# Optimization experiments

Measured on AMD Instinct MI355X. Metric: run time of the kernel, lower is better.

The kernel has to match this reference:

```python
import jax, jax.numpy as jnp
import numpy as np

HEAD = 8
PAD = (2, 2)   # (mod//2, mod//2 + mod%2) for dim=508, head=8 -> mod=4
EPS = 1e-6


def setup_inputs() -> dict:
    key = jax.random.key(0)
    ks = jax.random.split(key, 4)
    d_pad = 512  # 508 + mod(4)
    s = 1.0 / np.sqrt(d_pad).astype(np.float32)
    inp = jax.random.normal(ks[0], (2, 2048, 508), dtype=jnp.float32)
    Wq = jax.random.normal(ks[1], (d_pad, d_pad), dtype=jnp.float32) * s
    Wk = jax.random.normal(ks[2], (d_pad, d_pad), dtype=jnp.float32) * s
    Wv = jax.random.normal(ks[3], (d_pad, d_pad), dtype=jnp.float32) * s
    gamma = jnp.ones((d_pad,), dtype=jnp.float32)
    beta = jnp.zeros((d_pad,), dtype=jnp.float32)
    return {"inp": inp, "Wq": Wq, "Wk": Wk, "Wv": Wv, "gamma": gamma, "beta": beta}


def reference(inp, Wq, Wk, Wv, gamma, beta):
    # pad feature dim so it divides head count (torch F.pad on last dim)
    x = jnp.pad(inp, ((0, 0), (0, 0), (PAD[0], PAD[1])))  # [B, L, D]
    residual = x
    b, l, d = x.shape
    h = HEAD
    dh = d // h
    inv_sqrt_dh = 1.0 / np.sqrt(dh).astype(np.float32)

    def proj(W):
        # torch Linear (no bias): x @ W.T ; then split heads -> [B, H, L, dh]
        return (x @ W.T).reshape(b, l, h, dh).transpose(0, 2, 1, 3)

    q = proj(Wq)
    k = proj(Wk)
    v = proj(Wv)

    score = jnp.einsum('bhld,bhmd->bhlm', q, k) * inv_sqrt_dh  # [B,H,L,L]
    attn = jax.nn.softmax(score, axis=-1)
    out = jnp.einsum('bhlm,bhmd->bhld', attn, v)               # [B,H,L,dh]
    out = out.transpose(0, 2, 1, 3).reshape(b, l, d)           # unshape

    # dropout is identity in eval mode; residual + layernorm
    y = out + residual
    mu = jnp.mean(y, axis=-1, keepdims=True)
    var = jnp.mean(jnp.square(y - mu), axis=-1, keepdims=True)
    z = (y - mu) / jnp.sqrt(var + EPS)
    out = gamma * z + beta

    out = out[:, :, PAD[0]:-PAD[1]]  # strip padding back to original dim
    return out, attn
```

## Files before the change

kernel.cpp:

```cpp
#include <hip/hip_runtime.h>

typedef short bf16x8 __attribute__((ext_vector_type(8)));
typedef float f32x4 __attribute__((ext_vector_type(4)));
typedef unsigned short u16;
typedef u16 u16x8 __attribute__((ext_vector_type(8)));
typedef u16 u16x4 __attribute__((ext_vector_type(4)));

#define L_ 2048
#define D_ 512
#define H_ 8
#define DH_ 64
#define DIN 508
#define EXPC 0.18033688011112042f

static __device__ __forceinline__ u16 f2b(float f){
  unsigned u = __builtin_bit_cast(unsigned, f);
  unsigned r = u + 0x7fffu + ((u >> 16) & 1u);
  return (u16)(r >> 16);
}
static __device__ __forceinline__ float b2f(u16 u){
  unsigned x = ((unsigned)u) << 16;
  return __builtin_bit_cast(float, x);
}
static __device__ __forceinline__ bf16x8 asbf(u16x8 v){
  return __builtin_bit_cast(bf16x8, v);
}
#define MFMA16(a,b,c) __builtin_amdgcn_mfma_f32_16x16x32_bf16(a,b,c,0,0,0)

__global__ __launch_bounds__(512) void cvt_kernel(
    const float* __restrict__ inp, const float* __restrict__ Wq,
    const float* __restrict__ Wk, const float* __restrict__ Wv,
    u16* __restrict__ Xb, u16* __restrict__ Wb)
{
  const int tid = blockIdx.x*512 + threadIdx.x;
  if (tid < 262144) {
    const int idx8 = tid*8;
    const int row = idx8 >> 9, col = idx8 & 511;
    u16x8 o;
    #pragma unroll
    for (int e=0;e<8;++e){
      const int c = col+e;
      const float v = (c>=2 && c<510) ? inp[(size_t)row*DIN + (c-2)] : 0.f;
      o[e] = f2b(v);
    }
    *(u16x8*)&Xb[idx8] = o;
  } else {
    const int idx8 = (tid - 262144)*8;
    const int row = idx8 >> 9, col = idx8 & 511;
    const float* __restrict__ W = (row < 512) ? Wq : (row < 1024) ? Wk : Wv;
    const float* p = &W[(size_t)(row & 511)*D_ + col];
    u16x8 o;
    #pragma unroll
    for (int e=0;e<8;++e) o[e] = f2b(p[e]);
    *(u16x8*)&Wb[idx8] = o;
  }
}

__global__ __launch_bounds__(512) void proj_kernel(
    const u16* __restrict__ Xb, const u16* __restrict__ Wb,
    u16* __restrict__ Qg, u16* __restrict__ Kg, u16* __restrict__ Vt)
{
  __shared__ u16 Xl[128*72];
  __shared__ u16 Wl[128*72];
  const int t = threadIdx.x;
  const int lane = t & 63, wid = t >> 6;
  const int wr = wid >> 2, wc = wid & 3;
  const int i0 = blockIdx.x * 128;
  const int j0 = blockIdx.y * 128;
  const int mat = j0 >> 9;
  const int srow = t >> 3, sc8 = (t & 7) * 8;

  f32x4 acc[4][2];
  #pragma unroll
  for (int a=0;a<4;++a){
    #pragma unroll
    for (int bq=0;bq<2;++bq){ f32x4 z = {0.f,0.f,0.f,0.f}; acc[a][bq] = z; }
  }

  u16x8 xa0 = *(const u16x8*)&Xb[(size_t)(i0+srow)*D_ + sc8];
  u16x8 xa1 = *(const u16x8*)&Xb[(size_t)(i0+64+srow)*D_ + sc8];
  u16x8 wa0 = *(const u16x8*)&Wb[(size_t)(j0+srow)*D_ + sc8];
  u16x8 wa1 = *(const u16x8*)&Wb[(size_t)(j0+64+srow)*D_ + sc8];

  for (int kt=0; kt<8; ++kt){
    __syncthreads();
    *(u16x8*)&Xl[srow*72 + sc8] = xa0;
    *(u16x8*)&Xl[(64+srow)*72 + sc8] = xa1;
    *(u16x8*)&Wl[srow*72 + sc8] = wa0;
    *(u16x8*)&Wl[(64+srow)*72 + sc8] = wa1;
    __syncthreads();
    if (kt < 7){
      const int k1 = (kt+1)*64;
      xa0 = *(const u16x8*)&Xb[(size_t)(i0+srow)*D_ + k1 + sc8];
      xa1 = *(const u16x8*)&Xb[(size_t)(i0+64+srow)*D_ + k1 + sc8];
      wa0 = *(const u16x8*)&Wb[(size_t)(j0+srow)*D_ + k1 + sc8];
      wa1 = *(const u16x8*)&Wb[(size_t)(j0+64+srow)*D_ + k1 + sc8];
    }
    #pragma unroll
    for (int ks=0; ks<2; ++ks){
      const int ko = ks*32 + (lane>>4)*8;
      bf16x8 af[4], bfr[2];
      #pragma unroll
      for (int fm=0; fm<4; ++fm)
        af[fm] = *(const bf16x8*)&Xl[(wr*64 + fm*16 + (lane&15))*72 + ko];
      #pragma unroll
      for (int fn=0; fn<2; ++fn)
        bfr[fn] = *(const bf16x8*)&Wl[(wc*32 + fn*16 + (lane&15))*72 + ko];
      #pragma unroll
      for (int fm=0; fm<4; ++fm){
        #pragma unroll
        for (int fn=0; fn<2; ++fn)
          acc[fm][fn] = MFMA16(af[fm], bfr[fn], acc[fm][fn]);
      }
    }
  }
  #pragma unroll
  for (int fm=0; fm<4; ++fm){
    const int ibase = i0 + wr*64 + fm*16 + (lane>>4)*4;
    const int b = ibase >> 11;
    const int li = ibase & (L_-1);
    #pragma unroll
    for (int fn=0; fn<2; ++fn){
      const int n = j0 + wc*32 + fn*16 + (lane&15);
      const int h = (n>>6) & 7;
      const int dh = n & 63;
      if (mat == 2){
        u16x4 pk;
        #pragma unroll
        for (int r=0;r<4;++r) pk[r] = f2b(acc[fm][fn][r]);
        *(u16x4*)&Vt[((size_t)(b*H_+h)*DH_ + dh)*L_ + li] = pk;
      } else {
        u16* dst = ((mat==0)? Qg : Kg) + ((size_t)(b*H_+h)*L_ + li)*DH_ + dh;
        #pragma unroll
        for (int r=0;r<4;++r) dst[(size_t)r*DH_] = f2b(acc[fm][fn][r]);
      }
    }
  }
}

__global__ __launch_bounds__(512, 4) void attn_kernel(
    const u16* __restrict__ Qg, const u16* __restrict__ Kg,
    const u16* __restrict__ Vt, float* __restrict__ attn, float* __restrict__ Og)
{
  __shared__ u16 Vbuf[2][64*136];
  __shared__ u16 Pbuf[2][32*136];
  __shared__ float inv_rs[32];
  float* rsp = (float*)Vbuf;

  const int t = threadIdx.x, lane = t & 63, wid = t >> 6;
  const int lane15 = lane & 15, g = lane >> 4, g4 = g*8;
  const int lin = blockIdx.x;
  const int idx = lin >> 3;
  const int bh = (lin & 7) + 8*(idx & 1);
  const int q0 = (idx >> 1) * 32;
  const u16* Qp = Qg + ((size_t)bh*L_ + q0)*DH_;
  const u16* Kp = Kg + (size_t)bh*L_*DH_;
  const u16* Vp = Vt + (size_t)bh*DH_*L_;

  bf16x8 qf[2][2];
  #pragma unroll
  for (int qi=0;qi<2;++qi){
    #pragma unroll
    for (int ks=0;ks<2;++ks)
      qf[qi][ks] = *(const bf16x8*)&Qp[(size_t)(qi*16 + lane15)*DH_ + ks*32 + g4];
  }

  const int vr0 = t>>4, vcm = (t&15)*8;
  const int mrow = wid*16 + lane15;

  float racc0 = 0.f, racc1 = 0.f;
  {
    u16x8 nk0 = *(const u16x8*)&Kp[(size_t)mrow*DH_ + g4];
    u16x8 nk1 = *(const u16x8*)&Kp[(size_t)mrow*DH_ + 32 + g4];
    for (int kt=0; kt<16; ++kt){
      bf16x8 kf0 = asbf(nk0), kf1 = asbf(nk1);
      if (kt < 15){
        nk0 = *(const u16x8*)&Kp[(size_t)((kt+1)*128 + mrow)*DH_ + g4];
        nk1 = *(const u16x8*)&Kp[(size_t)((kt+1)*128 + mrow)*DH_ + 32 + g4];
      }
      f32x4 s0 = {0.f,0.f,0.f,0.f}, s1 = {0.f,0.f,0.f,0.f};
      s0 = MFMA16(kf0, qf[0][0], s0); s0 = MFMA16(kf1, qf[0][1], s0);
      s1 = MFMA16(kf0, qf[1][0], s1); s1 = MFMA16(kf1, qf[1][1], s1);
      #pragma unroll
      for (int r=0;r<4;++r){
        racc0 += exp2f(s0[r]*EXPC);
        racc1 += exp2f(s1[r]*EXPC);
      }
    }
  }
  racc0 += __shfl_xor(racc0, 16); racc0 += __shfl_xor(racc0, 32);
  racc1 += __shfl_xor(racc1, 16); racc1 += __shfl_xor(racc1, 32);
  if (lane < 16){ rsp[wid*32 + lane] = racc0; rsp[wid*32 + 16 + lane] = racc1; }
  __syncthreads();
  if (t < 32){
    float s = 0.f;
    #pragma unroll
    for (int w=0;w<8;++w) s += rsp[w*32 + t];
    inv_rs[t] = 1.f/s;
  }
  __syncthreads();

  const int qpv = wid>>2, d0 = (wid&3)*16;
  f32x4 o0 = {0.f,0.f,0.f,0.f}, o1 = {0.f,0.f,0.f,0.f};
  const int sr = t >> 4;
  const int sc4 = (t & 15) * 4;
  float* abase = attn + ((size_t)bh*L_ + q0 + sr)*L_ + sc4;
  const float sinv = inv_rs[sr];

  u16x8 k0 = *(const u16x8*)&Kp[(size_t)mrow*DH_ + g4];
  u16x8 k1 = *(const u16x8*)&Kp[(size_t)mrow*DH_ + 32 + g4];
  u16x8 va = *(const u16x8*)&Vp[(size_t)vr0*L_ + vcm];
  u16x8 vb = *(const u16x8*)&Vp[(size_t)(32+vr0)*L_ + vcm];

  {
    f32x4 s0 = {0.f,0.f,0.f,0.f}, s1 = {0.f,0.f,0.f,0.f};
    s0 = MFMA16(asbf(k0), qf[0][0], s0); s0 = MFMA16(asbf(k1), qf[0][1], s0);
    s1 = MFMA16(asbf(k0), qf[1][0], s1); s1 = MFMA16(asbf(k1), qf[1][1], s1);
    u16x4 p0, p1;
    #pragma unroll
    for (int r=0;r<4;++r){ p0[r] = f2b(exp2f(s0[r]*EXPC)); p1[r] = f2b(exp2f(s1[r]*EXPC)); }
    *(u16x4*)&Pbuf[0][lane15*136 + wid*16 + g*4] = p0;
    *(u16x4*)&Pbuf[0][(16 + lane15)*136 + wid*16 + g*4] = p1;
    *(u16x8*)&Vbuf[0][vr0*136 + vcm] = va;
    *(u16x8*)&Vbuf[0][(32+vr0)*136 + vcm] = vb;
  }
  __syncthreads();

  for (int kt=0; kt<16; ++kt){
    const int cur = kt & 1;
    if (kt < 15){
      k0 = *(const u16x8*)&Kp[(size_t)((kt+1)*128 + mrow)*DH_ + g4];
      k1 = *(const u16x8*)&Kp[(size_t)((kt+1)*128 + mrow)*DH_ + 32 + g4];
      va = *(const u16x8*)&Vp[(size_t)vr0*L_ + (kt+1)*128 + vcm];
      vb = *(const u16x8*)&Vp[(size_t)(32+vr0)*L_ + (kt+1)*128 + vcm];
    }
    {
      const u16x4 pva = *(const u16x4*)&Pbuf[cur][sr*136 + sc4];
      const u16x4 pvb = *(const u16x4*)&Pbuf[cur][sr*136 + 64 + sc4];
      f32x4 w0, w1;
      w0[0]=b2f(pva[0])*sinv; w0[1]=b2f(pva[1])*sinv;
      w0[2]=b2f(pva[2])*sinv; w0[3]=b2f(pva[3])*sinv;
      w1[0]=b2f(pvb[0])*sinv; w1[1]=b2f(pvb[1])*sinv;
      w1[2]=b2f(pvb[2])*sinv; w1[3]=b2f(pvb[3])*sinv;
      __builtin_nontemporal_store(w0, (f32x4*)&abase[kt*128]);
      __builtin_nontemporal_store(w1, (f32x4*)&abase[kt*128 + 64]);
    }
    #pragma unroll
    for (int ms=0; ms<4; ++ms){
      bf16x8 pa = *(const bf16x8*)&Pbuf[cur][(qpv*16 + lane15)*136 + ms*32 + g4];
      bf16x8 vv = *(const bf16x8*)&Vbuf[cur][(d0 + lane15)*136 + ms*32 + g4];
      if (ms&1) o1 = MFMA16(pa, vv, o1); else o0 = MFMA16(pa, vv, o0);
    }
    if (kt < 15){
      f32x4 s0 = {0.f,0.f,0.f,0.f}, s1 = {0.f,0.f,0.f,0.f};
      s0 = MFMA16(asbf(k0), qf[0][0], s0); s0 = MFMA16(asbf(k1), qf[0][1], s0);
      s1 = MFMA16(asbf(k0), qf[1][0], s1); s1 = MFMA16(asbf(k1), qf[1][1], s1);
      u16x4 p0, p1;
      #pragma unroll
      for (int r=0;r<4;++r){ p0[r] = f2b(exp2f(s0[r]*EXPC)); p1[r] = f2b(exp2f(s1[r]*EXPC)); }
      *(u16x4*)&Pbuf[cur^1][lane15*136 + wid*16 + g*4] = p0;
      *(u16x4*)&Pbuf[cur^1][(16 + lane15)*136 + wid*16 + g*4] = p1;
      *(u16x8*)&Vbuf[cur^1][vr0*136 + vcm] = va;
      *(u16x8*)&Vbuf[cur^1][(32+vr0)*136 + vcm] = vb;
    }
    __syncthreads();
  }
  {
    const int b = bh>>3, h = bh&7;
    #pragma unroll
    for (int r=0;r<4;++r){
      const int qr = qpv*16 + g*4 + r;
      Og[((size_t)(b*L_ + q0 + qr))*D_ + h*DH_ + d0 + lane15] = (o0[r]+o1[r])*inv_rs[qr];
    }
  }
}

__global__ __launch_bounds__(256) void ln_kernel(
    const float* __restrict__ Og, const float* __restrict__ inp,
    const float* __restrict__ gamma, const float* __restrict__ beta,
    float* __restrict__ out0)
{
  const int row = blockIdx.x, t = threadIdx.x;
  const int lane = t & 63, wid = t >> 6;
  const int c2 = t + 256;
  const float x1 = (t >= 2) ? inp[(size_t)row*DIN + t-2] : 0.f;
  const float x2 = (c2 < 510) ? inp[(size_t)row*DIN + c2-2] : 0.f;
  const float y1 = Og[(size_t)row*D_ + t]  + x1;
  const float y2 = Og[(size_t)row*D_ + c2] + x2;
  float s = y1 + y2, ss = y1*y1 + y2*y2;
  #pragma unroll
  for (int off=1; off<64; off<<=1){
    s  += __shfl_xor(s,  off);
    ss += __shfl_xor(ss, off);
  }
  __shared__ float red[4][2];
  if (lane == 0){ red[wid][0] = s; red[wid][1] = ss; }
  __syncthreads();
  s  = red[0][0]+red[1][0]+red[2][0]+red[3][0];
  ss = red[0][1]+red[1][1]+red[2][1]+red[3][1];
  const float mu   = s * (1.f/512.f);
  const float var  = ss * (1.f/512.f) - mu*mu;
  const float rstd = rsqrtf(var + 1e-6f);
  const float z1 = (y1 - mu)*rstd*gamma[t]  + beta[t];
  const float z2 = (y2 - mu)*rstd*gamma[c2] + beta[c2];
  if (t >= 2)   out0[(size_t)row*DIN + t-2]  = z1;
  if (c2 < 510) out0[(size_t)row*DIN + c2-2] = z2;
}

extern "C" void kernel_launch(void* const* d_in, const int* in_sizes, int n_in,
                              void* d_out, int out_size, void* d_ws, size_t ws_size,
                              hipStream_t stream) {
  const float* inp   = (const float*)d_in[0];
  const float* Wq    = (const float*)d_in[1];
  const float* Wk    = (const float*)d_in[2];
  const float* Wv    = (const float*)d_in[3];
  const float* gamma = (const float*)d_in[4];
  const float* beta  = (const float*)d_in[5];

  char* ws = (char*)d_ws;
  u16*   Qg = (u16*)(ws);
  u16*   Kg = (u16*)(ws + 4194304);
  u16*   Vt = (u16*)(ws + 8388608);
  float* Og = (float*)(ws + 12582912);
  u16*   Xb = (u16*)(ws + 12582912);
  u16*   Wb = (u16*)(ws + 16777216);

  float* out0 = (float*)d_out;
  float* attn = out0 + 2080768;

  cvt_kernel <<<704, 512, 0, stream>>>(inp, Wq, Wk, Wv, Xb, Wb);
  proj_kernel<<<dim3(32,12), 512, 0, stream>>>(Xb, Wb, Qg, Kg, Vt);
  attn_kernel<<<1024, 512, 0, stream>>>(Qg, Kg, Vt, attn, Og);
  ln_kernel  <<<4096, 256, 0, stream>>>(Og, inp, gamma, beta, out0);
}
```

Baseline: 132.6 us.

## Batch attention-probability stores into 512-column chunks with a wider P staging buffer

Replaces the double-buffered 128-column P and V tiles with a single 32x512 P staging buffer and one V tile. The normalized attention weights are written to global memory once every four key tiles, each warp storing four full rows of 512 columns. The goal is longer contiguous nontemporal store runs for the large attn output. In exchange the software pipelining between score computation and PV is lost, and each iteration now needs two or three barriers.

```diff
diff --git a/kernel.cpp b/kernel.cpp
--- a/kernel.cpp
+++ b/kernel.cpp
@@ -142,10 +142,10 @@
     const u16* __restrict__ Qg, const u16* __restrict__ Kg,
     const u16* __restrict__ Vt, float* __restrict__ attn, float* __restrict__ Og)
 {
-  __shared__ u16 Vbuf[2][64*136];
-  __shared__ u16 Pbuf[2][32*136];
+  __shared__ u16 P4[32*520];
+  __shared__ u16 Vl[64*136];
   __shared__ float inv_rs[32];
-  float* rsp = (float*)Vbuf;
+  float* rsp = (float*)P4;
 
   const int t = threadIdx.x, lane = t & 63, wid = t >> 6;
   const int lane15 = lane & 15, g = lane >> 4, g4 = g*8;
@@ -202,68 +202,59 @@
 
   const int qpv = wid>>2, d0 = (wid&3)*16;
   f32x4 o0 = {0.f,0.f,0.f,0.f}, o1 = {0.f,0.f,0.f,0.f};
-  const int sr = t >> 4;
-  const int sc4 = (t & 15) * 4;
-  float* abase = attn + ((size_t)bh*L_ + q0 + sr)*L_ + sc4;
-  const float sinv = inv_rs[sr];
 
   u16x8 k0 = *(const u16x8*)&Kp[(size_t)mrow*DH_ + g4];
   u16x8 k1 = *(const u16x8*)&Kp[(size_t)mrow*DH_ + 32 + g4];
   u16x8 va = *(const u16x8*)&Vp[(size_t)vr0*L_ + vcm];
   u16x8 vb = *(const u16x8*)&Vp[(size_t)(32+vr0)*L_ + vcm];
 
-  {
-    f32x4 s0 = {0.f,0.f,0.f,0.f}, s1 = {0.f,0.f,0.f,0.f};
-    s0 = MFMA16(asbf(k0), qf[0][0], s0); s0 = MFMA16(asbf(k1), qf[0][1], s0);
-    s1 = MFMA16(asbf(k0), qf[1][0], s1); s1 = MFMA16(asbf(k1), qf[1][1], s1);
-    u16x4 p0, p1;
-    #pragma unroll
-    for (int r=0;r<4;++r){ p0[r] = f2b(exp2f(s0[r]*EXPC)); p1[r] = f2b(exp2f(s1[r]*EXPC)); }
-    *(u16x4*)&Pbuf[0][lane15*136 + wid*16 + g*4] = p0;
-    *(u16x4*)&Pbuf[0][(16 + lane15)*136 + wid*16 + g*4] = p1;
-    *(u16x8*)&Vbuf[0][vr0*136 + vcm] = va;
-    *(u16x8*)&Vbuf[0][(32+vr0)*136 + vcm] = vb;
-  }
-  __syncthreads();
-
   for (int kt=0; kt<16; ++kt){
-    const int cur = kt & 1;
+    const int cbase = (kt & 3) * 128;
+    bf16x8 kf0 = asbf(k0), kf1 = asbf(k1);
     if (kt < 15){
       k0 = *(const u16x8*)&Kp[(size_t)((kt+1)*128 + mrow)*DH_ + g4];
       k1 = *(const u16x8*)&Kp[(size_t)((kt+1)*128 + mrow)*DH_ + 32 + g4];
+    }
+    f32x4 s0 = {0.f,0.f,0.f,0.f}, s1 = {0.f,0.f,0.f,0.f};
+    s0 = MFMA16(kf0, qf[0][0], s0); s0 = MFMA16(kf1, qf[0][1], s0);
+    s1 = MFMA16(kf0, qf[1][0], s1); s1 = MFMA16(kf1, qf[1][1], s1);
+    u16x4 p0, p1;
+    #pragma unroll
+    for (int r=0;r<4;++r){ p0[r] = f2b(exp2f(s0[r]*EXPC)); p1[r] = f2b(exp2f(s1[r]*EXPC)); }
+    *(u16x4*)&P4[lane15*520 + cbase + wid*16 + g*4] = p0;
+    *(u16x4*)&P4[(16 + lane15)*520 + cbase + wid*16 + g*4] = p1;
+    __syncthreads();
+    *(u16x8*)&Vl[vr0*136 + vcm] = va;
+    *(u16x8*)&Vl[(32+vr0)*136 + vcm] = vb;
+    if (kt < 15){
       va = *(const u16x8*)&Vp[(size_t)vr0*L_ + (kt+1)*128 + vcm];
       vb = *(const u16x8*)&Vp[(size_t)(32+vr0)*L_ + (kt+1)*128 + vcm];
     }
-    {
-      const u16x4 pva = *(const u16x4*)&Pbuf[cur][sr*136 + sc4];
-      const u16x4 pvb = *(const u16x4*)&Pbuf[cur][sr*136 + 64 + sc4];
-      f32x4 w0, w1;
-      w0[0]=b2f(pva[0])*sinv; w0[1]=b2f(pva[1])*sinv;
-      w0[2]=b2f(pva[2])*sinv; w0[3]=b2f(pva[3])*sinv;
-      w1[0]=b2f(pvb[0])*sinv; w1[1]=b2f(pvb[1])*sinv;
-      w1[2]=b2f(pvb[2])*sinv; w1[3]=b2f(pvb[3])*sinv;
-      __builtin_nontemporal_store(w0, (f32x4*)&abase[kt*128]);
-      __builtin_nontemporal_store(w1, (f32x4*)&abase[kt*128 + 64]);
-    }
+    __syncthreads();
     #pragma unroll
     for (int ms=0; ms<4; ++ms){
-      bf16x8 pa = *(const bf16x8*)&Pbuf[cur][(qpv*16 + lane15)*136 + ms*32 + g4];
-      bf16x8 vv = *(const bf16x8*)&Vbuf[cur][(d0 + lane15)*136 + ms*32 + g4];
+      bf16x8 pa = *(const bf16x8*)&P4[(qpv*16 + lane15)*520 + cbase + ms*32 + g4];
+      bf16x8 vv = *(const bf16x8*)&Vl[(d0 + lane15)*136 + ms*32 + g4];
       if (ms&1) o1 = MFMA16(pa, vv, o1); else o0 = MFMA16(pa, vv, o0);
     }
-    if (kt < 15){
-      f32x4 s0 = {0.f,0.f,0.f,0.f}, s1 = {0.f,0.f,0.f,0.f};
-      s0 = MFMA16(asbf(k0), qf[0][0], s0); s0 = MFMA16(asbf(k1), qf[0][1], s0);
-      s1 = MFMA16(asbf(k0), qf[1][0], s1); s1 = MFMA16(asbf(k1), qf[1][1], s1);
-      u16x4 p0, p1;
-      #pragma unroll
-      for (int r=0;r<4;++r){ p0[r] = f2b(exp2f(s0[r]*EXPC)); p1[r] = f2b(exp2f(s1[r]*EXPC)); }
-      *(u16x4*)&Pbuf[cur^1][lane15*136 + wid*16 + g*4] = p0;
-      *(u16x4*)&Pbuf[cur^1][(16 + lane15)*136 + wid*16 + g*4] = p1;
-      *(u16x8*)&Vbuf[cur^1][vr0*136 + vcm] = va;
-      *(u16x8*)&Vbuf[cur^1][(32+vr0)*136 + vcm] = vb;
-    }
-    __syncthreads();
+    if ((kt & 3) == 3){
+      const int mt = kt >> 2;
+      float* dst = attn + ((size_t)bh*L_ + q0 + wid*4)*L_ + mt*512 + lane*4;
+      #pragma unroll
+      for (int rr=0; rr<4; ++rr){
+        const float iv = inv_rs[wid*4 + rr];
+        const u16x4 pa = *(const u16x4*)&P4[(wid*4 + rr)*520 + lane*4];
+        const u16x4 pb = *(const u16x4*)&P4[(wid*4 + rr)*520 + 256 + lane*4];
+        f32x4 wa_, wb_;
+        wa_[0]=b2f(pa[0])*iv; wa_[1]=b2f(pa[1])*iv;
+        wa_[2]=b2f(pa[2])*iv; wa_[3]=b2f(pa[3])*iv;
+        wb_[0]=b2f(pb[0])*iv; wb_[1]=b2f(pb[1])*iv;
+        wb_[2]=b2f(pb[2])*iv; wb_[3]=b2f(pb[3])*iv;
+        __builtin_nontemporal_store(wa_, (f32x4*)&dst[(size_t)rr*L_]);
+        __builtin_nontemporal_store(wb_, (f32x4*)&dst[(size_t)rr*L_ + 256]);
+      }
+      __syncthreads();
+    }
   }
   {
     const int b = bh>>3, h = bh&7;
```

Result: no change. 134.7 us (+1.6%).
